# Kernel optimization log

Hardware: AMD Instinct MI355X
Metric: run time of the kernel (lower is better)

## Reference

```python
import jax, jax.numpy as jnp
import numpy as np

N = 100000   # nodes
E = 1600000  # edges
IN = 3       # in_channels
H = 32       # hidden_channels
C = 10       # num_classes_dynamic (== num output classes here)
G = 64       # number of graphs in the batch


def setup_inputs() -> dict:
    key = jax.random.key(0)
    ks = jax.random.split(key, 12)
    def w(k, shape, fan_in):
        return jax.random.normal(k, shape, jnp.float32) / np.sqrt(fan_in).astype(np.float32)
    inp = {}
    inp["x"] = jax.random.normal(ks[0], (N, IN), jnp.float32)
    inp["edge_index"] = jax.random.randint(ks[1], (2, E), 0, N, jnp.int32)
    inp["batch"] = jnp.sort(jax.random.randint(ks[2], (N,), 0, G, jnp.int32))
    # per-class linear filters (DynamicEdgeConv.filters)
    inp["filt_W"] = w(ks[3], (C, IN, H), IN)
    inp["filt_b"] = jnp.zeros((C, H), jnp.float32)
    # shared edge MLP: Linear(2H,H) -> ReLU -> Linear(H,H)
    inp["mlp_W1"] = w(ks[4], (2 * H, H), 2 * H)
    inp["mlp_b1"] = jnp.zeros((H,), jnp.float32)
    inp["mlp_W2"] = w(ks[5], (H, H), H)
    inp["mlp_b2"] = jnp.zeros((H,), jnp.float32)
    # GCN layers (gcn1 input dim hardcoded 323 = IN + C*H)
    inp["gcn1_W"] = w(ks[6], (IN + C * H, H), IN + C * H)
    inp["gcn1_b"] = jnp.zeros((H,), jnp.float32)
    inp["gcn2_W"] = w(ks[7], (H, H), H)
    inp["gcn2_b"] = jnp.zeros((H,), jnp.float32)
    # classifier
    inp["cls_W"] = w(ks[8], (H, C), H)
    inp["cls_b"] = jnp.zeros((C,), jnp.float32)
    return inp


def _gcn_conv(x, W, b, row, col, dinv):
    # PyG GCNConv: add self-loops, sym-normalize, aggregate src->dst
    xw = x @ W                                   # [N, H]
    norm = dinv[row] * dinv[col]                 # [E]
    out = jax.ops.segment_sum(xw[row] * norm[:, None], col, num_segments=x.shape[0])
    out = out + xw * (dinv * dinv)[:, None]      # self-loop term, norm = 1/deg_i
    return out + b


def _forward(x, edge_index, batch, filt_W, filt_b, mlp_W1, mlp_b1, mlp_W2, mlp_b2,
             gcn1_W, gcn1_b, gcn2_W, gcn2_b, cls_W, cls_b):
    row, col = edge_index[0], edge_index[1]
    n = x.shape[0]

    # DynamicEdgeConv: per-class filter -> gather(row,col) -> edge MLP -> scatter_add into col
    def per_class(_, wb):
        Wc, bc = wb
        xc = x @ Wc + bc                                      # [N, H]
        ef = jnp.concatenate([xc[row], xc[col]], axis=1)      # [E, 2H]
        h = jax.nn.relu(ef @ mlp_W1 + mlp_b1) @ mlp_W2 + mlp_b2
        return None, jax.ops.segment_sum(h, col, num_segments=n)
    _, aggs = jax.lax.scan(per_class, None, (filt_W, filt_b))  # [C, N, H]

    feat = jnp.concatenate([x, aggs.transpose(1, 0, 2).reshape(n, -1)], axis=1)  # [N, IN + C*H]

    deg = jax.ops.segment_sum(jnp.ones(row.shape[0], x.dtype), col, num_segments=n) + 1.0
    dinv = deg ** -0.5
    h1 = jax.nn.relu(_gcn_conv(feat, gcn1_W, gcn1_b, row, col, dinv))
    h2 = jax.nn.relu(_gcn_conv(h1, gcn2_W, gcn2_b, row, col, dinv))

    counts = jax.ops.segment_sum(jnp.ones(n, x.dtype), batch, num_segments=G)
    pooled = jax.ops.segment_sum(h2, batch, num_segments=G) / jnp.maximum(counts, 1.0)[:, None]
    return pooled @ cls_W + cls_b                             # [G, C]


def reference(x, edge_index, batch, filt_W, filt_b, mlp_W1, mlp_b1, mlp_W2, mlp_b2,
              gcn1_W, gcn1_b, gcn2_W, gcn2_b, cls_W, cls_b):
    return _forward(x, edge_index, batch, filt_W, filt_b, mlp_W1, mlp_b1, mlp_W2, mlp_b2,
                    gcn1_W, gcn1_b, gcn2_W, gcn2_b, cls_W, cls_b)
```

## Files before the change

### kernel.cpp

```cpp
#include <hip/hip_runtime.h>

#define NN 100000
#define NE 1600000
#define HH 32
#define CC 10
#define GG 64
#define NB 391
#define PBLK 100
#define ECH 16000
#define MTOT (NB * PBLK)
#define MSB ((MTOT + 255) / 256)

typedef _Float16 half8 __attribute__((ext_vector_type(8)));
typedef _Float16 half2v __attribute__((ext_vector_type(2)));
typedef float f32x4 __attribute__((ext_vector_type(4)));

__device__ __forceinline__ half2v bch(int v) { return __builtin_bit_cast(half2v, v); }

__global__ void zero_f(float* p, int n) {
    int i = blockIdx.x * 256 + threadIdx.x;
    if (i < n) p[i] = 0.0f;
}

__global__ void precompute_small(const float* __restrict__ fW, const float* __restrict__ fb,
                                 const float* __restrict__ W1, const float* __restrict__ b1,
                                 const float* __restrict__ W2, const float* __restrict__ b2,
                                 const float* __restrict__ g1W, float* __restrict__ tab) {
    int c = blockIdx.x;
    int k = threadIdx.x >> 5;
    int j = threadIdx.x & 31;
    float m = 0.f;
    for (int mm = 0; mm < 32; ++mm)
        m += W2[k * 32 + mm] * g1W[(3 + 32 * c + mm) * 32 + j];
    tab[2240 + c * 1024 + k * 32 + j] = m;

    if (k < 3) {
        float a = 0.f, b = 0.f;
        for (int i = 0; i < 32; ++i) {
            float w = fW[c * 96 + k * 32 + i];
            a += w * W1[i * 32 + j];
            b += w * W1[(32 + i) * 32 + j];
        }
        tab[c * 96 + k * 32 + j] = a;
        tab[960 + c * 96 + k * 32 + j] = b;
    } else if (k == 3) {
        float h = b1[j];
        for (int i = 0; i < 32; ++i)
            h += fb[c * 32 + i] * (W1[i * 32 + j] + W1[(32 + i) * 32 + j]);
        tab[1920 + c * 32 + j] = h;
    } else if (k == 4 && c == 0) {
        float t = 0.f;
        for (int cc2 = 0; cc2 < CC; ++cc2)
            for (int mm = 0; mm < 32; ++mm)
                t += b2[mm] * g1W[(3 + 32 * cc2 + mm) * 32 + j];
        tab[12480 + j] = t;
    }
}

__global__ void mfrag_kernel(const float* __restrict__ tab, _Float16* __restrict__ Mfrag) {
    int gid = blockIdx.x * 256 + threadIdx.x;
    if (gid >= 1280) return;
    int set = gid >> 6, l = gid & 63;
    int kc = set >> 1, jt = set & 1;
    int j = jt * 16 + (l & 15);
    int kbase = kc * 32 + (l >> 4) * 8;
#pragma unroll
    for (int i = 0; i < 8; ++i)
        Mfrag[gid * 8 + i] = (_Float16)tab[2240 + (kbase + i) * 32 + j];
}

__global__ void bucket_hist(const int* __restrict__ ei, int* __restrict__ mat) {
    __shared__ int h[NB];
    int blk = blockIdx.x, tid = threadIdx.x;
    for (int i = tid; i < NB; i += 256) h[i] = 0;
    __syncthreads();
    int base = blk * ECH;
    for (int k = tid; k < ECH; k += 256)
        atomicAdd(&h[ei[NE + base + k] >> 8], 1);
    __syncthreads();
    for (int i = tid; i < NB; i += 256) mat[i * PBLK + blk] = h[i];
}

__global__ void scan_m1(const int* __restrict__ mat, int* __restrict__ msum) {
    __shared__ int sh[256];
    int b = blockIdx.x, t = threadIdx.x;
    int i = b * 256 + t;
    sh[t] = (i < MTOT) ? mat[i] : 0;
    __syncthreads();
    for (int off = 128; off > 0; off >>= 1) {
        if (t < off) sh[t] += sh[t + off];
        __syncthreads();
    }
    if (t == 0) msum[b] = sh[0];
}

__global__ void scan_m2(int* __restrict__ msum) {
    __shared__ int sh[256];
    int t = threadIdx.x;
    int v = (t < MSB) ? msum[t] : 0;
    sh[t] = v;
    __syncthreads();
    for (int off = 1; off < 256; off <<= 1) {
        int add = (t >= off) ? sh[t - off] : 0;
        __syncthreads();
        sh[t] += add;
        __syncthreads();
    }
    if (t < MSB) msum[t] = sh[t] - v;
}

__global__ void scan_m3(int* __restrict__ mat, const int* __restrict__ msum) {
    __shared__ int sh[256];
    int b = blockIdx.x, t = threadIdx.x;
    int i = b * 256 + t;
    int v = (i < MTOT) ? mat[i] : 0;
    sh[t] = v;
    __syncthreads();
    for (int off = 1; off < 256; off <<= 1) {
        int add = (t >= off) ? sh[t - off] : 0;
        __syncthreads();
        sh[t] += add;
        __syncthreads();
    }
    if (i < MTOT) mat[i] = sh[t] - v + msum[b];
}

__global__ void bucket_scatter(const int* __restrict__ ei, const int* __restrict__ mat,
                               unsigned int* __restrict__ part) {
    __shared__ int bas[NB];
    __shared__ int cur[NB];
    int blk = blockIdx.x, tid = threadIdx.x;
    for (int i = tid; i < NB; i += 256) { bas[i] = mat[i * PBLK + blk]; cur[i] = 0; }
    __syncthreads();
    int base = blk * ECH;
    for (int k = tid; k < ECH; k += 256) {
        int e = base + k;
        int r = ei[e];
        int c = ei[NE + e];
        int b = c >> 8;
        int local = atomicAdd(&cur[b], 1);
        part[bas[b] + local] = (unsigned)r | ((unsigned)(c & 255) << 24);
    }
}

__global__ void bucket_build(const unsigned int* __restrict__ part, const int* __restrict__ mat,
                             const float* __restrict__ x, int* __restrict__ csr_row,
                             int* __restrict__ ideg, int* __restrict__ offs,
                             float* __restrict__ dinv, float4* __restrict__ xpad,
                             uint4* __restrict__ xs) {
    __shared__ int lh[256];
    __shared__ int lex[256];
    __shared__ int cur[256];
    int b = blockIdx.x, tid = threadIdx.x;
    int ebase = mat[b * PBLK];
    int eend = (b == NB - 1) ? NE : mat[(b + 1) * PBLK];
    int m = eend - ebase;
    lh[tid] = 0;
    __syncthreads();
    for (int k = tid; k < m; k += 256) {
        unsigned v = part[ebase + k];
        atomicAdd(&lh[v >> 24], 1);
    }
    __syncthreads();
    int cnt = lh[tid];
    lex[tid] = cnt;
    __syncthreads();
    for (int off = 1; off < 256; off <<= 1) {
        int v = (tid >= off) ? lex[tid - off] : 0;
        __syncthreads();
        lex[tid] += v;
        __syncthreads();
    }
    int excl = lex[tid] - cnt;
    lex[tid] = excl;
    cur[tid] = 0;
    int n = b * 256 + tid;
    if (n < NN) {
        ideg[n] = cnt;
        offs[n] = ebase + excl;
        float di = rsqrtf((float)cnt + 1.0f);
        dinv[n] = di;
        float x0 = x[n * 3], x1 = x[n * 3 + 1], x2 = x[n * 3 + 2];
        xpad[n] = make_float4(x0, x1, x2, di);
        _Float16 hx = (_Float16)x0, hy = (_Float16)x1, hz = (_Float16)x2;
        half2v sx = {hx, hx}, sy = {hy, hy}, sz = {hz, hz};
        xs[n] = make_uint4(__builtin_bit_cast(unsigned int, sx),
                           __builtin_bit_cast(unsigned int, sy),
                           __builtin_bit_cast(unsigned int, sz), 0u);
    }
    if (b == 0 && tid == 0) offs[NN] = NE;
    __syncthreads();
    for (int k = tid; k < m; k += 256) {
        unsigned v = part[ebase + k];
        int cl = (int)(v >> 24);
        int r = (int)(v & 0x00FFFFFFu);
        int local = atomicAdd(&cur[cl], 1);
        csr_row[ebase + lex[cl] + local] = r;
    }
}

__global__ __launch_bounds__(256, 6) void edgeconv_fused(
    const uint4* __restrict__ xs, const int* __restrict__ offs,
    const int* __restrict__ csr_row, const float* __restrict__ tab,
    _Float16* __restrict__ aggh) {
    int lane = threadIdx.x & 63;
    int j = lane & 31;
    int half = lane >> 5;

    half2v A0[5], A1[5], A2[5], B0[5], B1[5], B2[5], hb[5];
#pragma unroll
    for (int p = 0; p < 5; ++p) {
        int c0 = 2 * p, c1 = 2 * p + 1;
        A0[p] = half2v{(_Float16)tab[c0 * 96 + j],        (_Float16)tab[c1 * 96 + j]};
        A1[p] = half2v{(_Float16)tab[c0 * 96 + 32 + j],   (_Float16)tab[c1 * 96 + 32 + j]};
        A2[p] = half2v{(_Float16)tab[c0 * 96 + 64 + j],   (_Float16)tab[c1 * 96 + 64 + j]};
        B0[p] = half2v{(_Float16)tab[960 + c0 * 96 + j],      (_Float16)tab[960 + c1 * 96 + j]};
        B1[p] = half2v{(_Float16)tab[960 + c0 * 96 + 32 + j], (_Float16)tab[960 + c1 * 96 + 32 + j]};
        B2[p] = half2v{(_Float16)tab[960 + c0 * 96 + 64 + j], (_Float16)tab[960 + c1 * 96 + 64 + j]};
        hb[p] = half2v{(_Float16)tab[1920 + c0 * 32 + j], (_Float16)tab[1920 + c1 * 32 + j]};
    }
    const half2v zero = half2v{(_Float16)0.f, (_Float16)0.f};

    int wid = blockIdx.x * 4 + (threadIdx.x >> 6);
    const int wstride = gridDim.x * 4;

    for (int n = wid; n < NN; n += wstride) {
        uint4 qn = xs[n];
        half2v pxn = bch((int)qn.x), pyn = bch((int)qn.y), pzn = bch((int)qn.z);
        half2v va[5], acc[5];
        float accf[10];
#pragma unroll
        for (int p = 0; p < 5; ++p) {
            va[p] = hb[p] + pxn * B0[p] + pyn * B1[p] + pzn * B2[p];
            acc[p] = zero;
            accf[2 * p] = 0.f;
            accf[2 * p + 1] = 0.f;
        }
        int e0 = offs[n], e1 = offs[n + 1];
        for (int base = e0; base < e1; base += 64) {
            int ee = base + lane;
            int r = (ee < e1) ? csr_row[ee] : 0;
            uint4 q = xs[r];
            int c2 = e1 - base;
            if (c2 > 64) c2 = 64;
            int tfull = c2 >> 1;
            int t = 0;
            for (; t + 4 <= tfull; t += 4) {
#pragma unroll
                for (int u = 0; u < 4; ++u) {
                    int src = 2 * (t + u) + half;
                    half2v px = bch(__shfl((int)q.x, src, 64));
                    half2v py = bch(__shfl((int)q.y, src, 64));
                    half2v pz = bch(__shfl((int)q.z, src, 64));
#pragma unroll
                    for (int p = 0; p < 5; ++p) {
                        half2v v = va[p] + px * A0[p] + py * A1[p] + pz * A2[p];
                        v = __builtin_elementwise_max(v, zero);
                        acc[p] += v;
                    }
                }
#pragma unroll
                for (int p = 0; p < 5; ++p) {
                    accf[2 * p]     += (float)acc[p].x;
                    accf[2 * p + 1] += (float)acc[p].y;
                    acc[p] = zero;
                }
            }
            for (; t < tfull; ++t) {
                int src = 2 * t + half;
                half2v px = bch(__shfl((int)q.x, src, 64));
                half2v py = bch(__shfl((int)q.y, src, 64));
                half2v pz = bch(__shfl((int)q.z, src, 64));
#pragma unroll
                for (int p = 0; p < 5; ++p) {
                    half2v v = va[p] + px * A0[p] + py * A1[p] + pz * A2[p];
                    v = __builtin_elementwise_max(v, zero);
                    acc[p] += v;
                }
            }
            if (c2 & 1) {
                int src = c2 - 1;
                half2v px = bch(__shfl((int)q.x, src, 64));
                half2v py = bch(__shfl((int)q.y, src, 64));
                half2v pz = bch(__shfl((int)q.z, src, 64));
                if (half == 0) {
#pragma unroll
                    for (int p = 0; p < 5; ++p) {
                        half2v v = va[p] + px * A0[p] + py * A1[p] + pz * A2[p];
                        v = __builtin_elementwise_max(v, zero);
                        acc[p] += v;
                    }
                }
            }
#pragma unroll
            for (int p = 0; p < 5; ++p) {
                accf[2 * p]     += (float)acc[p].x;
                accf[2 * p + 1] += (float)acc[p].y;
                acc[p] = zero;
            }
        }
#pragma unroll
        for (int c = 0; c < 10; ++c) accf[c] += __shfl_xor(accf[c], 32, 64);
        _Float16* arow = aggh + (size_t)n * 320 + j;
#pragma unroll
        for (int i = 0; i < 5; ++i) {
            int c = half * 5 + i;
            arow[c * 32] = (_Float16)accf[c];
        }
    }
}

__global__ __launch_bounds__(256) void fold_mfma(
    const _Float16* __restrict__ aggh, const _Float16* __restrict__ MfragG,
    const float4* __restrict__ xpad, const int* __restrict__ ideg,
    const float* __restrict__ tab, const float* __restrict__ g1W,
    _Float16* __restrict__ y1) {
    __shared__ _Float16 Mf[10240];
    {
        const uint4* src = (const uint4*)MfragG;
        uint4* dst = (uint4*)Mf;
        for (int i = threadIdx.x; i < 1280; i += 256) dst[i] = src[i];
    }
    __syncthreads();

    int wave = blockIdx.x * 4 + (threadIdx.x >> 6);
    int lane = threadIdx.x & 63;
    int n0 = wave * 16;
    if (n0 >= NN) return;

    int m = lane & 15, q = lane >> 4;
    int arow_n = n0 + m;
    bool rowok = arow_n < NN;
    const _Float16* arow = aggh + (size_t)arow_n * 320 + q * 8;

    const half8* mf = (const half8*)Mf;
    f32x4 acc0 = {0.f, 0.f, 0.f, 0.f};
    f32x4 acc1 = {0.f, 0.f, 0.f, 0.f};

    for (int kc = 0; kc < 10; ++kc) {
        half8 a;
        if (rowok) a = *(const half8*)(arow + kc * 32);
        else {
#pragma unroll
            for (int i = 0; i < 8; ++i) a[i] = (_Float16)0.f;
        }
        half8 b0 = mf[(kc * 2 + 0) * 64 + lane];
        half8 b1 = mf[(kc * 2 + 1) * 64 + lane];
        acc0 = __builtin_amdgcn_mfma_f32_16x16x32_f16(a, b0, acc0, 0, 0, 0);
        acc1 = __builtin_amdgcn_mfma_f32_16x16x32_f16(a, b1, acc1, 0, 0, 0);
    }

    int jcol = lane & 15;
    float t0 = tab[12480 + jcol],      t1 = tab[12480 + 16 + jcol];
    float w00 = g1W[jcol],      w01 = g1W[32 + jcol],      w02 = g1W[64 + jcol];
    float w10 = g1W[16 + jcol], w11 = g1W[48 + jcol],      w12 = g1W[80 + jcol];
#pragma unroll
    for (int r = 0; r < 4; ++r) {
        int node = n0 + q * 4 + r;
        if (node < NN) {
            float4 xn = xpad[node];
            float dg = (float)ideg[node];
            float v0 = dg * t0 + xn.x * w00 + xn.y * w01 + xn.z * w02 + acc0[r];
            float v1 = dg * t1 + xn.x * w10 + xn.y * w11 + xn.z * w12 + acc1[r];
            y1[node * 32 + jcol]      = (_Float16)(v0 * xn.w);
            y1[node * 32 + 16 + jcol] = (_Float16)(v1 * xn.w);
        }
    }
}

__global__ __launch_bounds__(256, 8) void prop1_fused(
    const int* __restrict__ offs, const int* __restrict__ csr_row,
    const unsigned int* __restrict__ y1p, const float* __restrict__ dinv,
    const float* __restrict__ g1b, const float* __restrict__ g2W,
    unsigned int* __restrict__ y2p) {
    __shared__ float g2s[1024];
    for (int i = threadIdx.x; i < 1024; i += 256) g2s[i] = g2W[i];
    __syncthreads();

    int lane = threadIdx.x & 63;
    int l = lane & 15;
    int wid = blockIdx.x * 4 + (threadIdx.x >> 6);
    int n = wid * 4 + (lane >> 4);
    if (n >= NN) return;

    int e0 = offs[n], e1 = offs[n + 1];
    float sAl = 0.f, sAh = 0.f, sBl = 0.f, sBh = 0.f;
    int e = e0;
    for (; e + 7 < e1; e += 8) {
        int r[8];
#pragma unroll
        for (int u = 0; u < 8; ++u) r[u] = csr_row[e + u];
        half2v p[8];
#pragma unroll
        for (int u = 0; u < 8; ++u) p[u] = __builtin_bit_cast(half2v, y1p[r[u] * 16 + l]);
#pragma unroll
        for (int u = 0; u < 8; u += 2) {
            sAl += (float)p[u].x;     sAh += (float)p[u].y;
            sBl += (float)p[u + 1].x; sBh += (float)p[u + 1].y;
        }
    }
    if (e + 3 < e1) {
        int r[4];
#pragma unroll
        for (int u = 0; u < 4; ++u) r[u] = csr_row[e + u];
        half2v p[4];
#pragma unroll
        for (int u = 0; u < 4; ++u) p[u] = __builtin_bit_cast(half2v, y1p[r[u] * 16 + l]);
        sAl += (float)p[0].x + (float)p[2].x; sAh += (float)p[0].y + (float)p[2].y;
        sBl += (float)p[1].x + (float)p[3].x; sBh += (float)p[1].y + (float)p[3].y;
        e += 4;
    }
    if (e + 1 < e1) {
        int r0 = csr_row[e], r1 = csr_row[e + 1];
        half2v p0 = __builtin_bit_cast(half2v, y1p[r0 * 16 + l]);
        half2v p1 = __builtin_bit_cast(half2v, y1p[r1 * 16 + l]);
        sAl += (float)p0.x; sAh += (float)p0.y;
        sBl += (float)p1.x; sBh += (float)p1.y;
        e += 2;
    }
    if (e < e1) {
        int r = csr_row[e];
        half2v p = __builtin_bit_cast(half2v, y1p[r * 16 + l]);
        sAl += (float)p.x; sAh += (float)p.y;
    }
    float di = dinv[n];
    half2v pn = __builtin_bit_cast(half2v, y1p[n * 16 + l]);
    float h1l = di * (sAl + sBl + (float)pn.x);
    float h1h = di * (sAh + sBh + (float)pn.y);
    float hl = fmaxf(h1l + g1b[2 * l], 0.f);
    float hh = fmaxf(h1h + g1b[2 * l + 1], 0.f);

    float al = 0.f, ah = 0.f;
    int base = lane & 48;
#pragma unroll
    for (int m = 0; m < 16; ++m) {
        float xl = __shfl(hl, base + m, 64);
        float xh2 = __shfl(hh, base + m, 64);
        al += xl * g2s[(2 * m) * 32 + 2 * l] + xh2 * g2s[(2 * m + 1) * 32 + 2 * l];
        ah += xl * g2s[(2 * m) * 32 + 2 * l + 1] + xh2 * g2s[(2 * m + 1) * 32 + 2 * l + 1];
    }
    half2v o = {(_Float16)(al * di), (_Float16)(ah * di)};
    y2p[n * 16 + l] = __builtin_bit_cast(unsigned int, o);
}

__global__ __launch_bounds__(256, 8) void prop2_plain(
    const int* __restrict__ offs, const int* __restrict__ csr_row,
    const unsigned int* __restrict__ y2p, const float* __restrict__ dinv,
    unsigned int* __restrict__ outp) {
    int lane = threadIdx.x & 63;
    int l = lane & 15;
    int wid = blockIdx.x * 4 + (threadIdx.x >> 6);
    int n = wid * 4 + (lane >> 4);
    if (n >= NN) return;

    int e0 = offs[n], e1 = offs[n + 1];
    float sAl = 0.f, sAh = 0.f, sBl = 0.f, sBh = 0.f;
    int e = e0;
    for (; e + 7 < e1; e += 8) {
        int r[8];
#pragma unroll
        for (int u = 0; u < 8; ++u) r[u] = csr_row[e + u];
        half2v p[8];
#pragma unroll
        for (int u = 0; u < 8; ++u) p[u] = __builtin_bit_cast(half2v, y2p[r[u] * 16 + l]);
#pragma unroll
        for (int u = 0; u < 8; u += 2) {
            sAl += (float)p[u].x;     sAh += (float)p[u].y;
            sBl += (float)p[u + 1].x; sBh += (float)p[u + 1].y;
        }
    }
    if (e + 3 < e1) {
        int r[4];
#pragma unroll
        for (int u = 0; u < 4; ++u) r[u] = csr_row[e + u];
        half2v p[4];
#pragma unroll
        for (int u = 0; u < 4; ++u) p[u] = __builtin_bit_cast(half2v, y2p[r[u] * 16 + l]);
        sAl += (float)p[0].x + (float)p[2].x; sAh += (float)p[0].y + (float)p[2].y;
        sBl += (float)p[1].x + (float)p[3].x; sBh += (float)p[1].y + (float)p[3].y;
        e += 4;
    }
    if (e + 1 < e1) {
        int r0 = csr_row[e], r1 = csr_row[e + 1];
        half2v p0 = __builtin_bit_cast(half2v, y2p[r0 * 16 + l]);
        half2v p1 = __builtin_bit_cast(half2v, y2p[r1 * 16 + l]);
        sAl += (float)p0.x; sAh += (float)p0.y;
        sBl += (float)p1.x; sBh += (float)p1.y;
        e += 2;
    }
    if (e < e1) {
        int r = csr_row[e];
        half2v p = __builtin_bit_cast(half2v, y2p[r * 16 + l]);
        sAl += (float)p.x; sAh += (float)p.y;
    }
    float di = dinv[n];
    half2v pn = __builtin_bit_cast(half2v, y2p[n * 16 + l]);
    half2v o = {(_Float16)(di * (sAl + sBl + (float)pn.x)),
                (_Float16)(di * (sAh + sBh + (float)pn.y))};
    outp[n * 16 + l] = __builtin_bit_cast(unsigned int, o);
}

__global__ void pool_seg(const _Float16* __restrict__ h2, const float* __restrict__ g2b,
                         const int* __restrict__ batch, float* __restrict__ pooled,
                         float* __restrict__ counts) {
    int grp = threadIdx.x >> 5, j = threadIdx.x & 31;
    int base = (blockIdx.x * 8 + grp) * 64;
    if (base >= NN) return;
    float bj = g2b[j];
    float acc = 0.f, cnt = 0.f;
    int curg = -1;
    int lim = base + 64;
    if (lim > NN) lim = NN;
    for (int n = base; n < lim; ++n) {
        int g = batch[n];
        if (g != curg) {
            if (curg >= 0) {
                atomicAdd(&pooled[curg * 32 + j], acc);
                if (j == 0) atomicAdd(&counts[curg], cnt);
            }
            curg = g; acc = 0.f; cnt = 0.f;
        }
        acc += fmaxf((float)h2[n * 32 + j] + bj, 0.f);
        cnt += 1.f;
    }
    if (curg >= 0) {
        atomicAdd(&pooled[curg * 32 + j], acc);
        if (j == 0) atomicAdd(&counts[curg], cnt);
    }
}

__global__ void final_kernel(const float* __restrict__ pooled, const float* __restrict__ counts,
                             const float* __restrict__ clsW, const float* __restrict__ clsb,
                             float* __restrict__ out) {
    int tid = threadIdx.x;
    if (tid >= GG * CC) return;
    int g = tid / CC, cc = tid % CC;
    float inv = 1.0f / fmaxf(counts[g], 1.0f);
    float s = clsb[cc];
    for (int j = 0; j < 32; ++j) s += (pooled[g * 32 + j] * inv) * clsW[j * CC + cc];
    out[g * CC + cc] = s;
}

extern "C" void kernel_launch(void* const* d_in, const int* in_sizes, int n_in,
                              void* d_out, int out_size, void* d_ws, size_t ws_size,
                              hipStream_t stream) {
    const float* x     = (const float*)d_in[0];
    const int*   ei    = (const int*)d_in[1];
    const int*   batch = (const int*)d_in[2];
    const float* fW    = (const float*)d_in[3];
    const float* fb    = (const float*)d_in[4];
    const float* W1    = (const float*)d_in[5];
    const float* b1    = (const float*)d_in[6];
    const float* W2    = (const float*)d_in[7];
    const float* b2    = (const float*)d_in[8];
    const float* g1W   = (const float*)d_in[9];
    const float* g1b   = (const float*)d_in[10];
    const float* g2W   = (const float*)d_in[11];
    const float* g2b   = (const float*)d_in[12];
    const float* clsW  = (const float*)d_in[13];
    const float* clsb  = (const float*)d_in[14];
    float* out = (float*)d_out;

    float4*         xpad    = (float4*)d_ws;
    uint4*          xs      = (uint4*)(xpad + NN);
    _Float16*       aggh    = (_Float16*)(xs + NN);
    unsigned int*   part    = (unsigned int*)aggh;
    int*            csr_row = (int*)(aggh + (size_t)NN * 320);
    int*            mat     = (int*)(csr_row + NE);
    int*            msum    = mat + MTOT;
    int*            ideg    = msum + 256;
    int*            offs    = ideg + NN;
    float*          dinv    = (float*)(offs + NN + 1);
    float*          tab     = dinv + NN;
    _Float16*       Mfrag   = (_Float16*)(tab + 16384);
    _Float16*       y1      = Mfrag + 10240;
    unsigned int*   y2p     = (unsigned int*)(y1 + (size_t)NN * 32);
    unsigned int*   h2p     = y2p + (size_t)NN * 16;
    float*          pooled  = (float*)(h2p + (size_t)NN * 16);
    float*          counts  = pooled + GG * 32;

    const int propBlocks = (NN + 15) / 16;
    const int foldBlocks = ((NN + 15) / 16 + 3) / 4;

    zero_f<<<(GG * 33 + 255) / 256, 256, 0, stream>>>(pooled, GG * 33);
    precompute_small<<<10, 1024, 0, stream>>>(fW, fb, W1, b1, W2, b2, g1W, tab);
    mfrag_kernel<<<5, 256, 0, stream>>>(tab, Mfrag);

    bucket_hist<<<PBLK, 256, 0, stream>>>(ei, mat);
    scan_m1<<<MSB, 256, 0, stream>>>(mat, msum);
    scan_m2<<<1, 256, 0, stream>>>(msum);
    scan_m3<<<MSB, 256, 0, stream>>>(mat, msum);
    bucket_scatter<<<PBLK, 256, 0, stream>>>(ei, mat, part);
    bucket_build<<<NB, 256, 0, stream>>>(part, mat, x, csr_row, ideg, offs, dinv, xpad, xs);

    edgeconv_fused<<<2048, 256, 0, stream>>>(xs, offs, csr_row, tab, aggh);
    fold_mfma<<<foldBlocks, 256, 0, stream>>>(aggh, Mfrag, xpad, ideg, tab, g1W, y1);

    prop1_fused<<<propBlocks, 256, 0, stream>>>(offs, csr_row, (const unsigned int*)y1,
                                                dinv, g1b, g2W, y2p);
    prop2_plain<<<propBlocks, 256, 0, stream>>>(offs, csr_row, y2p, dinv, h2p);
    pool_seg<<<(NN + 511) / 512, 256, 0, stream>>>((const _Float16*)h2p, g2b, batch,
                                                   pooled, counts);
    final_kernel<<<1, 640, 0, stream>>>(pooled, counts, clsW, clsb, out);
}
```

Before: 380.9 us.

## Software-pipeline edge gathers across nodes in edgeconv and propagation kernels

Restructures the edgeconv node loop so each wave prefetches the next node's offsets, features and first chunk of neighbor rows (or the next chunk within a high-degree node) while computing the current chunk. The propagation kernels likewise prefetch the next batch of CSR indices while the current gathered values are summed. The goal is to hide the dependent-load latency of the index-then-gather chain. In exchange it uses more registers, so edgeconv's occupancy hint drops from 6 to 4 waves, and the aggregate writes become nontemporal stores.

Measured after the change: 368.8 us. 1.03x faster.

```diff
diff --git a/kernel.cpp b/kernel.cpp
--- a/kernel.cpp
+++ b/kernel.cpp
@@ -199,7 +199,51 @@
     }
 }
 
-__global__ __launch_bounds__(256, 6) void edgeconv_fused(
+#define EC_PAIR(QQ, SRC) do { \
+    half2v px_ = bch(__shfl((int)(QQ).x, (SRC), 64)); \
+    half2v py_ = bch(__shfl((int)(QQ).y, (SRC), 64)); \
+    half2v pz_ = bch(__shfl((int)(QQ).z, (SRC), 64)); \
+    _Pragma("unroll") \
+    for (int p = 0; p < 5; ++p) { \
+        half2v v = va[p] + px_ * A0[p] + py_ * A1[p] + pz_ * A2[p]; \
+        v = __builtin_elementwise_max(v, zero); \
+        acc[p] += v; \
+    } } while (0)
+
+#define EC_FLUSH() do { \
+    _Pragma("unroll") \
+    for (int p = 0; p < 5; ++p) { \
+        accf[2 * p]     += (float)acc[p].x; \
+        accf[2 * p + 1] += (float)acc[p].y; \
+        acc[p] = zero; \
+    } } while (0)
+
+#define EC_CHUNK_FROM(T0, QQ, C2) do { \
+    int tfull_ = (C2) >> 1; \
+    int t_ = (T0); \
+    for (; t_ + 4 <= tfull_; t_ += 4) { \
+        _Pragma("unroll") \
+        for (int u = 0; u < 4; ++u) EC_PAIR(QQ, 2 * (t_ + u) + half); \
+        EC_FLUSH(); \
+    } \
+    for (; t_ < tfull_; ++t_) EC_PAIR(QQ, 2 * t_ + half); \
+    if ((C2) & 1) { \
+        int src_ = (C2) - 1; \
+        half2v px_ = bch(__shfl((int)(QQ).x, src_, 64)); \
+        half2v py_ = bch(__shfl((int)(QQ).y, src_, 64)); \
+        half2v pz_ = bch(__shfl((int)(QQ).z, src_, 64)); \
+        if (half == 0) { \
+            _Pragma("unroll") \
+            for (int p = 0; p < 5; ++p) { \
+                half2v v = va[p] + px_ * A0[p] + py_ * A1[p] + pz_ * A2[p]; \
+                v = __builtin_elementwise_max(v, zero); \
+                acc[p] += v; \
+            } \
+        } \
+    } \
+    EC_FLUSH(); } while (0)
+
+__global__ __launch_bounds__(256, 4) void edgeconv_fused(
     const uint4* __restrict__ xs, const int* __restrict__ offs,
     const int* __restrict__ csr_row, const float* __restrict__ tab,
     _Float16* __restrict__ aggh) {
@@ -222,10 +266,36 @@
     const half2v zero = half2v{(_Float16)0.f, (_Float16)0.f};
 
     int wid = blockIdx.x * 4 + (threadIdx.x >> 6);
-    const int wstride = gridDim.x * 4;
-
-    for (int n = wid; n < NN; n += wstride) {
-        uint4 qn = xs[n];
+    const int ws = gridDim.x * 4;
+
+    int n = wid;
+    if (n >= NN) return;
+    int e0 = offs[n];
+    int e1 = offs[n + 1];
+    uint4 qn = xs[n];
+    int n2 = n + ws;
+    int e0n = 0, e1n = 0;
+    if (n2 < NN) { e0n = offs[n2]; e1n = offs[n2 + 1]; }
+    uint4 q;
+    {
+        int ee = e0 + lane;
+        int r0 = (ee < e1) ? csr_row[ee] : 0;
+        q = xs[r0];
+    }
+
+    while (true) {
+        int n3 = n2 + ws;
+        int e0n2 = 0, e1n2 = 0;
+        if (n3 < NN) { e0n2 = offs[n3]; e1n2 = offs[n3 + 1]; }
+        uint4 qn2 = make_uint4(0u, 0u, 0u, 0u);
+        if (n2 < NN) qn2 = xs[n2];
+
+        bool multi = (e1 - e0) > 64;
+        int pb = multi ? (e0 + 64) : e0n;
+        int pe = multi ? e1 : e1n;
+        int ee2 = pb + lane;
+        int rn = (ee2 < pe) ? csr_row[ee2] : 0;
+
         half2v pxn = bch((int)qn.x), pyn = bch((int)qn.y), pzn = bch((int)qn.z);
         half2v va[5], acc[5];
         float accf[10];
@@ -236,77 +306,56 @@
             accf[2 * p] = 0.f;
             accf[2 * p + 1] = 0.f;
         }
-        int e0 = offs[n], e1 = offs[n + 1];
-        for (int base = e0; base < e1; base += 64) {
-            int ee = base + lane;
-            int r = (ee < e1) ? csr_row[ee] : 0;
-            uint4 q = xs[r];
-            int c2 = e1 - base;
-            if (c2 > 64) c2 = 64;
-            int tfull = c2 >> 1;
-            int t = 0;
-            for (; t + 4 <= tfull; t += 4) {
-#pragma unroll
-                for (int u = 0; u < 4; ++u) {
-                    int src = 2 * (t + u) + half;
-                    half2v px = bch(__shfl((int)q.x, src, 64));
-                    half2v py = bch(__shfl((int)q.y, src, 64));
-                    half2v pz = bch(__shfl((int)q.z, src, 64));
-#pragma unroll
-                    for (int p = 0; p < 5; ++p) {
-                        half2v v = va[p] + px * A0[p] + py * A1[p] + pz * A2[p];
-                        v = __builtin_elementwise_max(v, zero);
-                        acc[p] += v;
-                    }
-                }
-#pragma unroll
-                for (int p = 0; p < 5; ++p) {
-                    accf[2 * p]     += (float)acc[p].x;
-                    accf[2 * p + 1] += (float)acc[p].y;
-                    acc[p] = zero;
-                }
+
+        int c2 = e1 - e0;
+        if (c2 > 64) c2 = 64;
+        int t0 = 0;
+        if ((c2 >> 1) >= 4) {
+#pragma unroll
+            for (int u = 0; u < 4; ++u) EC_PAIR(q, 2 * u + half);
+            EC_FLUSH();
+            t0 = 4;
+        }
+        uint4 qpre = xs[rn];
+        EC_CHUNK_FROM(t0, q, c2);
+
+        if (multi) {
+            int base = e0 + 64;
+            uint4 qc = qpre;
+            while (true) {
+                int cc = e1 - base;
+                if (cc > 64) cc = 64;
+                int nb = base + 64;
+                bool m2 = nb < e1;
+                int pb2 = m2 ? nb : e0n;
+                int pe2 = m2 ? e1 : e1n;
+                int ee3 = pb2 + lane;
+                int rn2 = (ee3 < pe2) ? csr_row[ee3] : 0;
+                uint4 qp2 = xs[rn2];
+                EC_CHUNK_FROM(0, qc, cc);
+                qc = qp2;
+                if (!m2) break;
+                base = nb;
             }
-            for (; t < tfull; ++t) {
-                int src = 2 * t + half;
-                half2v px = bch(__shfl((int)q.x, src, 64));
-                half2v py = bch(__shfl((int)q.y, src, 64));
-                half2v pz = bch(__shfl((int)q.z, src, 64));
-#pragma unroll
-                for (int p = 0; p < 5; ++p) {
-                    half2v v = va[p] + px * A0[p] + py * A1[p] + pz * A2[p];
-                    v = __builtin_elementwise_max(v, zero);
-                    acc[p] += v;
-                }
-            }
-            if (c2 & 1) {
-                int src = c2 - 1;
-                half2v px = bch(__shfl((int)q.x, src, 64));
-                half2v py = bch(__shfl((int)q.y, src, 64));
-                half2v pz = bch(__shfl((int)q.z, src, 64));
-                if (half == 0) {
-#pragma unroll
-                    for (int p = 0; p < 5; ++p) {
-                        half2v v = va[p] + px * A0[p] + py * A1[p] + pz * A2[p];
-                        v = __builtin_elementwise_max(v, zero);
-                        acc[p] += v;
-                    }
-                }
-            }
-#pragma unroll
-            for (int p = 0; p < 5; ++p) {
-                accf[2 * p]     += (float)acc[p].x;
-                accf[2 * p + 1] += (float)acc[p].y;
-                acc[p] = zero;
-            }
-        }
+            qpre = qc;
+        }
+
 #pragma unroll
         for (int c = 0; c < 10; ++c) accf[c] += __shfl_xor(accf[c], 32, 64);
         _Float16* arow = aggh + (size_t)n * 320 + j;
 #pragma unroll
         for (int i = 0; i < 5; ++i) {
             int c = half * 5 + i;
-            arow[c * 32] = (_Float16)accf[c];
-        }
+            __builtin_nontemporal_store((_Float16)accf[c], arow + c * 32);
+        }
+
+        if (n2 >= NN) return;
+        n = n2;
+        n2 = n3;
+        e0 = e0n; e1 = e1n;
+        e0n = e0n2; e1n = e1n2;
+        qn = qn2;
+        q = qpre;
     }
 }
 
@@ -386,17 +435,27 @@
     int e0 = offs[n], e1 = offs[n + 1];
     float sAl = 0.f, sAh = 0.f, sBl = 0.f, sBh = 0.f;
     int e = e0;
-    for (; e + 7 < e1; e += 8) {
+    if (e + 7 < e1) {
         int r[8];
 #pragma unroll
         for (int u = 0; u < 8; ++u) r[u] = csr_row[e + u];
-        half2v p[8];
-#pragma unroll
-        for (int u = 0; u < 8; ++u) p[u] = __builtin_bit_cast(half2v, y1p[r[u] * 16 + l]);
-#pragma unroll
-        for (int u = 0; u < 8; u += 2) {
-            sAl += (float)p[u].x;     sAh += (float)p[u].y;
-            sBl += (float)p[u + 1].x; sBh += (float)p[u + 1].y;
+        while (true) {
+            half2v p[8];
+#pragma unroll
+            for (int u = 0; u < 8; ++u) p[u] = __builtin_bit_cast(half2v, y1p[r[u] * 16 + l]);
+            int e2 = e + 8;
+            bool more = (e2 + 7 < e1);
+            if (more) {
+#pragma unroll
+                for (int u = 0; u < 8; ++u) r[u] = csr_row[e2 + u];
+            }
+#pragma unroll
+            for (int u = 0; u < 8; u += 2) {
+                sAl += (float)p[u].x;     sAh += (float)p[u].y;
+                sBl += (float)p[u + 1].x; sBh += (float)p[u + 1].y;
+            }
+            e = e2;
+            if (!more) break;
         }
     }
     if (e + 3 < e1) {
@@ -456,17 +515,27 @@
     int e0 = offs[n], e1 = offs[n + 1];
     float sAl = 0.f, sAh = 0.f, sBl = 0.f, sBh = 0.f;
     int e = e0;
-    for (; e + 7 < e1; e += 8) {
+    if (e + 7 < e1) {
         int r[8];
 #pragma unroll
         for (int u = 0; u < 8; ++u) r[u] = csr_row[e + u];
-        half2v p[8];
-#pragma unroll
-        for (int u = 0; u < 8; ++u) p[u] = __builtin_bit_cast(half2v, y2p[r[u] * 16 + l]);
-#pragma unroll
-        for (int u = 0; u < 8; u += 2) {
-            sAl += (float)p[u].x;     sAh += (float)p[u].y;
-            sBl += (float)p[u + 1].x; sBh += (float)p[u + 1].y;
+        while (true) {
+            half2v p[8];
+#pragma unroll
+            for (int u = 0; u < 8; ++u) p[u] = __builtin_bit_cast(half2v, y2p[r[u] * 16 + l]);
+            int e2 = e + 8;
+            bool more = (e2 + 7 < e1);
+            if (more) {
+#pragma unroll
+                for (int u = 0; u < 8; ++u) r[u] = csr_row[e2 + u];
+            }
+#pragma unroll
+            for (int u = 0; u < 8; u += 2) {
+                sAl += (float)p[u].x;     sAh += (float)p[u].y;
+                sBl += (float)p[u + 1].x; sBh += (float)p[u + 1].y;
+            }
+            e = e2;
+            if (!more) break;
         }
     }
     if (e + 3 < e1) {
```
